# Kernel optimization log

Measured on AMD Instinct MI355X. Metric: run time of the kernel, lower is better.

The kernel has to match this reference:

```python
import jax, jax.numpy as jnp
import numpy as np

D_MODEL = 512
N_HEADS = 8
NUM_NODES = 20
EPS = 1e-5

def _layer_norm(x, g, b):
    mu = jnp.mean(x, axis=-1, keepdims=True)
    var = jnp.var(x, axis=-1, keepdims=True)
    return (x - mu) * jax.lax.rsqrt(var + EPS) * g + b

def _conv1d(x_bcn, w_oik):
    # x: [B, C, N], w: [O, I, K], padding = K//2 (same)
    k = w_oik.shape[-1]
    p = k // 2
    return jax.lax.conv_general_dilated(
        x_bcn, w_oik, window_strides=(1,), padding=[(p, p)],
        dimension_numbers=('NCH', 'OIH', 'NCH'))

def setup_inputs() -> dict:
    key = jax.random.key(0)
    ks = jax.random.split(key, 6)
    B, N, D, H = 4096, NUM_NODES, D_MODEL, N_HEADS
    x = jax.random.normal(ks[0], (B, N, D), dtype=jnp.float32)
    s = 1.0 / np.sqrt(D * 3)
    Wq = jax.random.normal(ks[1], (D, D, 3), dtype=jnp.float32) * s
    Wk = jax.random.normal(ks[2], (D, D, 3), dtype=jnp.float32) * s
    Wv = jax.random.normal(ks[3], (D, D, 3), dtype=jnp.float32) * s
    rel_table = jax.random.normal(ks[4], (2 * N - 1, H), dtype=jnp.float32) * 0.02
    Wo = jax.random.normal(ks[5], (D, D), dtype=jnp.float32) * (1.0 / np.sqrt(D))
    bo = jnp.zeros((D,), dtype=jnp.float32)
    ones = jnp.ones((D,), dtype=jnp.float32)
    zeros = jnp.zeros((D,), dtype=jnp.float32)
    return {"x": x, "Wq": Wq, "Wk": Wk, "Wv": Wv,
            "lnq_g": ones, "lnq_b": zeros, "lnk_g": ones, "lnk_b": zeros,
            "lnv_g": ones, "lnv_b": zeros,
            "rel_table": rel_table, "Wo": Wo, "bo": bo}

def reference(x, Wq, Wk, Wv, lnq_g, lnq_b, lnk_g, lnk_b, lnv_g, lnv_b, rel_table, Wo, bo):
    B, N, D = x.shape
    H = N_HEADS
    dk = D // H
    x_p = jnp.transpose(x, (0, 2, 1))  # [B, D, N]

    def proj(W, g, b):
        c = _conv1d(x_p, W)                      # [B, D, N]
        c = _layer_norm(jnp.transpose(c, (0, 2, 1)), g, b)  # [B, N, D]
        return x + c                              # residual

    q = proj(Wq, lnq_g, lnq_b)
    k = proj(Wk, lnk_g, lnk_b)
    v = proj(Wv, lnv_g, lnv_b)

    q = q.reshape(B, N, H, dk).transpose(0, 2, 1, 3)  # [B,H,N,dk]
    k = k.reshape(B, N, H, dk).transpose(0, 2, 1, 3)
    v = v.reshape(B, N, H, dk).transpose(0, 2, 1, 3)

    scale = 1.0 / np.sqrt(dk)
    scores = jnp.einsum('bhnd,bhmd->bhnm', q, k) * scale  # [B,H,N,N]

    # relative position bias: index[i,j] = i - j + N - 1
    coords = jnp.arange(N)
    rel_idx = coords[:, None] - coords[None, :] + (N - 1)   # [N,N]
    rel_bias = rel_table[rel_idx]                            # [N,N,H]
    rel_bias = jnp.transpose(rel_bias, (2, 0, 1))[None]      # [1,H,N,N]
    scores = scores + rel_bias

    attn = jax.nn.softmax(scores, axis=-1)
    out = jnp.einsum('bhnm,bhmd->bhnd', attn, v)             # [B,H,N,dk]
    out = out.transpose(0, 2, 1, 3).reshape(B, N, D)
    return out @ Wo.T + bo
```

## Files before the change

kernel.cpp:

```cpp
#include <hip/hip_runtime.h>
#include <hip/hip_bf16.h>
#include <stdint.h>
#include <string.h>

typedef __attribute__((ext_vector_type(8))) __bf16 bf16x8;
typedef __attribute__((ext_vector_type(4))) __bf16 bf16x4;
typedef __attribute__((ext_vector_type(4))) float f32x4;
typedef __attribute__((ext_vector_type(16))) float f32x16;

#define B_TOT   4096
#define NN      20
#define DM      512
#define NC1     1536
#define M_TOT   (B_TOT*NN)
#define NPAD    22

__device__ __forceinline__ void async_copy16(const __bf16* g, __bf16* l) {
    __builtin_amdgcn_global_load_lds(
        (__attribute__((address_space(1))) void*)g,
        (__attribute__((address_space(3))) void*)l, 16, 0, 0);
}

template<typename T>
__device__ __forceinline__ void load8(const T* p, float* r) {
    if constexpr (sizeof(T) == 4) {
        f32x4 a = *(const f32x4*)p;
        f32x4 b = *(const f32x4*)(p + 4);
#pragma unroll
        for (int i = 0; i < 4; ++i) { r[i] = a[i]; r[i + 4] = b[i]; }
    } else {
        bf16x8 a = *(const bf16x8*)p;
#pragma unroll
        for (int i = 0; i < 8; ++i) r[i] = (float)a[i];
    }
}

__device__ __forceinline__ bf16x8 zero8() {
    bf16x8 z;
#pragma unroll
    for (int i = 0; i < 8; ++i) z[i] = (__bf16)0.f;
    return z;
}

__device__ __forceinline__ uint32_t pkbf(float a, float b) {
    __bf16 x = (__bf16)a, y = (__bf16)b;
    uint16_t ux, uy;
    __builtin_memcpy(&ux, &x, 2); __builtin_memcpy(&uy, &y, 2);
    return (uint32_t)ux | ((uint32_t)uy << 16);
}

__device__ __forceinline__ bf16x8 mkfrag(uint32_t w0, uint32_t w1, uint32_t w2, uint32_t w3) {
    union { uint32_t u[4]; bf16x8 v; } X;
    X.u[0] = w0; X.u[1] = w1; X.u[2] = w2; X.u[3] = w3;
    return X.v;
}

__global__ void detect_kernel(const uint32_t* __restrict__ xw, int* __restrict__ mode) {
    int lane = threadIdx.x & 63;
    int susp = 0;
#pragma unroll
    for (int i = 0; i < 4; ++i) {
        uint32_t w = xw[lane * 4 + i];
        uint32_t e = (w >> 7) & 0xFF;
        if ((e >= 118 && e <= 130) || (w & 0xFFFFu) == 0) susp++;
    }
#pragma unroll
    for (int o = 32; o > 0; o >>= 1) susp += __shfl_xor(susp, o, 64);
    if (lane == 0) *mode = (susp > 128) ? 1 : 0;
}

template<typename T>
__device__ __forceinline__ void wt_body(
    const T* __restrict__ Wq, const T* __restrict__ Wk, const T* __restrict__ Wv,
    const T* __restrict__ Wo, __bf16* __restrict__ Wt, __bf16* __restrict__ Wob, int t)
{
    if (t < 3 * 512 * 512) {
        int p = t >> 18;
        int r = t & 262143;
        int o = r >> 9, i = r & 511;
        const T* W = (p == 0) ? Wq : ((p == 1) ? Wk : Wv);
        const T* src = W + (size_t)(o * 512 + i) * 3;
        float w0 = (float)src[0], w1 = (float)src[1], w2 = (float)src[2];
        size_t base = (size_t)(p * 512 + o) * 1536 + i;
        Wt[base]        = (__bf16)w0;
        Wt[base + 512]  = (__bf16)w1;
        Wt[base + 1024] = (__bf16)w2;
    } else {
        int g2 = t - 3 * 512 * 512;
        Wob[g2] = (__bf16)(float)Wo[g2];
    }
}

__global__ __launch_bounds__(256) void wt_kernel(
    const void* Wq, const void* Wk, const void* Wv, const void* Wo,
    __bf16* Wt, __bf16* Wob, const int* mode)
{
    int t = blockIdx.x * 256 + threadIdx.x;
    if (*mode)
        wt_body<__bf16>((const __bf16*)Wq, (const __bf16*)Wk, (const __bf16*)Wv,
                        (const __bf16*)Wo, Wt, Wob, t);
    else
        wt_body<float>((const float*)Wq, (const float*)Wk, (const float*)Wv,
                       (const float*)Wo, Wt, Wob, t);
}

template<typename T>
__device__ __forceinline__ void xpad_body(
    const T* __restrict__ x, __bf16* __restrict__ xp, int idx)
{
    int col = (idx & 63) * 8;
    int row = idx >> 6;
    int b = row / 22;
    int np = row - b * 22;
    bf16x8 ov;
    if (np == 0 || np == 21) {
        ov = zero8();
    } else {
        float tmp[8];
        load8<T>(x + ((size_t)(b * 20 + np - 1) * 512 + col), tmp);
#pragma unroll
        for (int t = 0; t < 8; ++t) ov[t] = (__bf16)tmp[t];
    }
    *(bf16x8*)(xp + (size_t)row * 512 + col) = ov;
}

__global__ __launch_bounds__(256) void xpad_kernel(
    const void* x, __bf16* xp, const int* mode)
{
    int idx = blockIdx.x * 256 + threadIdx.x;
    if (*mode) xpad_body<__bf16>((const __bf16*)x, xp, idx);
    else       xpad_body<float>((const float*)x, xp, idx);
}

#define SBAR()  __builtin_amdgcn_s_barrier()
#define SCHED0() __builtin_amdgcn_sched_barrier(0)
#define LGKM0() do { asm volatile("s_waitcnt lgkmcnt(0)" ::: "memory"); SCHED0(); } while (0)
#define VM4()   do { SCHED0(); asm volatile("s_waitcnt vmcnt(4)" ::: "memory"); } while (0)
#define VM0()   do { SCHED0(); asm volatile("s_waitcnt vmcnt(0)" ::: "memory"); } while (0)

__device__ __forceinline__ void g1_loadA(const __bf16* slab, int off, bf16x8 (&aq)[4]) {
#pragma unroll
    for (int i = 0; i < 4; ++i) aq[i] = *(const bf16x8*)(slab + off + i * 512);
}
__device__ __forceinline__ void g1_loadB(const __bf16* slab, int off, bf16x8 (&bq)[4]) {
#pragma unroll
    for (int i = 0; i < 4; ++i) bq[i] = *(const bf16x8*)(slab + off + i * 512);
}
template<int QM>
__device__ __forceinline__ void g1_mma(bf16x8 (&aq)[4], bf16x8 (&bq)[4], f32x4 (&acc)[8][4]) {
    __builtin_amdgcn_s_setprio(1);
#pragma unroll
    for (int i = 0; i < 4; ++i)
#pragma unroll
        for (int nf = 0; nf < 4; ++nf)
            acc[QM * 4 + i][nf] = __builtin_amdgcn_mfma_f32_16x16x32_bf16(
                aq[i], bq[nf], acc[QM * 4 + i][nf], 0, 0, 0);
    __builtin_amdgcn_s_setprio(0);
}

template<int NT>
__device__ __forceinline__ void kloop8(
    const __bf16* aP0, const __bf16* aP1, const __bf16* bP0, const __bf16* bP1,
    __bf16* shA, __bf16* shB, int sdst, int rdA, int rdB, f32x4 (&acc)[8][4])
{
    bf16x8 aq[4], bq[4];
    { __bf16* d = shA + 0 * 8192 + sdst; async_copy16(aP0 + 0, d);  async_copy16(aP1 + 0, d + 4096); }
    { __bf16* d = shB + 0 * 8192 + sdst; async_copy16(bP0 + 0, d);  async_copy16(bP1 + 0, d + 4096); }
    { __bf16* d = shA + 1 * 8192 + sdst; async_copy16(aP0 + 32, d); async_copy16(aP1 + 32, d + 4096); }
    { __bf16* d = shB + 1 * 8192 + sdst; async_copy16(bP0 + 32, d); async_copy16(bP1 + 32, d + 4096); }
    VM4();
    SBAR();

    for (int t = 0; t < NT; ++t) {
        const int cur = t & 1;
        const __bf16* A0 = shA + (cur * 2 + 0) * 8192;
        const __bf16* A1 = shA + (cur * 2 + 1) * 8192;
        const __bf16* B0 = shB + (cur * 2 + 0) * 8192;
        const __bf16* B1 = shB + (cur * 2 + 1) * 8192;
        __bf16* dA0 = shA + ((cur ^ 1) * 2 + 0) * 8192 + sdst;
        __bf16* dA1 = shA + ((cur ^ 1) * 2 + 1) * 8192 + sdst;
        __bf16* dB0 = shB + ((cur ^ 1) * 2 + 0) * 8192 + sdst;
        __bf16* dB1 = shB + ((cur ^ 1) * 2 + 1) * 8192 + sdst;
        const int kn = (t + 1) * 64;
        const bool st = (t < NT - 1);

        g1_loadA(A0, rdA, aq);
        g1_loadB(B0, rdB, bq);
        if (st) { async_copy16(aP0 + kn, dA0); async_copy16(aP1 + kn, dA0 + 4096); }
        SBAR(); LGKM0();
        g1_mma<0>(aq, bq, acc);
        SBAR();

        g1_loadA(A0, rdA + 2048, aq);
        if (st) { async_copy16(bP0 + kn, dB0); async_copy16(bP1 + kn, dB0 + 4096); }
        if (st) VM4(); else VM0();
        SBAR(); LGKM0();
        g1_mma<1>(aq, bq, acc);
        SBAR();

        g1_loadA(A1, rdA, aq);
        g1_loadB(B1, rdB, bq);
        if (st) { async_copy16(aP0 + kn + 32, dA1); async_copy16(aP1 + kn + 32, dA1 + 4096); }
        SBAR(); LGKM0();
        g1_mma<0>(aq, bq, acc);
        SBAR();

        g1_loadA(A1, rdA + 2048, aq);
        if (st) { async_copy16(bP0 + kn + 32, dB1); async_copy16(bP1 + kn + 32, dB1 + 4096); }
        if (st) VM4();
        SBAR(); LGKM0();
        g1_mma<1>(aq, bq, acc);
        SBAR();
    }
}

__global__ __launch_bounds__(512, 2) void g1_kernel(
    const __bf16* __restrict__ xpad, const __bf16* __restrict__ Wt,
    __bf16* __restrict__ Cout, int mbase)
{
    extern __shared__ __align__(16) __bf16 sh[];
    __bf16* shA = sh;
    __bf16* shB = sh + 32768;

    const int tid = threadIdx.x;
    const int w = tid >> 6, l = tid & 63;
    const int lr = l & 15, lq = l >> 4;
    const int wm = w >> 2, wn = w & 3;

    int nwg = gridDim.x;
    int bid = blockIdx.x;
    if ((nwg & 7) == 0) bid = (bid & 7) * (nwg >> 3) + (bid >> 3);
    const int nb = bid % 6;
    const int mb = bid / 6;
    const int n0 = nb * 256;
    const int mloc = mb * 256;

    const int rin = l >> 2;
    const int pc  = (l & 3) * 8;
    const int lc  = (rin >= 8) ? (pc ^ 16) : pc;
    const int R0 = w * 16 + rin;
    const int R1 = 128 + R0;
    const int g0 = mbase + mloc + R0, g1r = mbase + mloc + R1;
    const __bf16* aP0 = xpad + (size_t)((g0 / 20) * 22 + g0 % 20) * 512 + lc;
    const __bf16* aP1 = xpad + (size_t)((g1r / 20) * 22 + g1r % 20) * 512 + lc;
    const __bf16* bP0 = Wt + (size_t)(n0 + R0) * 1536 + lc;
    const __bf16* bP1 = Wt + (size_t)(n0 + R1) * 1536 + lc;
    const int sdst = w * 512 + l * 8;

    const int swzcol = (lr >= 8) ? ((lq * 8) ^ 16) : (lq * 8);
    const int ardoff = lr * 32 + swzcol;
    const int rdA = wm * 8 * 512 + ardoff;
    const int rdB = wn * 4 * 512 + ardoff;

    f32x4 acc[8][4] = {};
    kloop8<24>(aP0, aP1, bP0, bP1, shA, shB, sdst, rdA, rdB, acc);

#pragma unroll
    for (int mf = 0; mf < 8; ++mf) {
#pragma unroll
        for (int r = 0; r < 4; ++r) {
            int row = mloc + wm * 128 + mf * 16 + lq * 4 + r;
            size_t base = (size_t)row * 1536 + n0 + wn * 64 + lr;
#pragma unroll
            for (int nf = 0; nf < 4; ++nf)
                Cout[base + nf * 16] = (__bf16)acc[mf][nf][r];
        }
    }
}

template<typename T>
__device__ __forceinline__ void attn_body(
    const __bf16* __restrict__ xpad, const __bf16* __restrict__ cqkv,
    const T* __restrict__ lnq_g, const T* __restrict__ lnq_b,
    const T* __restrict__ lnk_g, const T* __restrict__ lnk_b,
    const T* __restrict__ lnv_g, const T* __restrict__ lnv_b,
    const T* __restrict__ rel, __bf16* __restrict__ aout, int bbase,
    __bf16* sq , __bf16* vT ,
    float* rbt )
{
    const int tid = threadIdx.x;
    const int wave = tid >> 6, lane = tid & 63;
    const int bl = blockIdx.x;
    char* sqb = (char*)sq;
    char* vTb = (char*)vT;
    const size_t xpbase = ((size_t)(bbase + bl) * NPAD + 1) * DM;
    const size_t cbase = (size_t)bl * NN * NC1;

#pragma unroll
    for (int k = 0; k < 4; ++k)
        *(bf16x8*)(vTb + tid * 64 + k * 16) = zero8();
    if (tid < 312) {
        int h = tid & 7, d = tid >> 3;
        rbt[h * 40 + d] = (float)rel[tid];
    }
    __syncthreads();

#pragma unroll
    for (int rr = 0; rr < 8; ++rr) {
        int row = wave + rr * 8;
        if (row < 60) {
            int p = row / 20;
            int n = row - p * 20;
            bf16x8 cv = *(const bf16x8*)(cqkv + cbase + (size_t)n * NC1 + p * 512 + lane * 8);
            bf16x8 xv = *(const bf16x8*)(xpad + xpbase + (size_t)n * DM + lane * 8);
            float vals[8]; float s1 = 0.f, s2 = 0.f;
#pragma unroll
            for (int t = 0; t < 8; ++t) { float f = (float)cv[t]; vals[t] = f; s1 += f; s2 += f * f; }
#pragma unroll
            for (int o = 32; o > 0; o >>= 1) { s1 += __shfl_xor(s1, o, 64); s2 += __shfl_xor(s2, o, 64); }
            float mu = s1 * (1.f / 512.f);
            float var = s2 * (1.f / 512.f) - mu * mu;
            float rs = rsqrtf(var + 1e-5f);
            const T* g  = (p == 0) ? lnq_g : (p == 1) ? lnk_g : lnv_g;
            const T* bb = (p == 0) ? lnq_b : (p == 1) ? lnk_b : lnv_b;
            float gv[8], bv[8];
            load8<T>(g  + lane * 8, gv);
            load8<T>(bb + lane * 8, bv);
            bf16x8 ov;
#pragma unroll
            for (int t = 0; t < 8; ++t)
                ov[t] = (__bf16)((vals[t] - mu) * rs * gv[t] + bv[t] + (float)xv[t]);
            if (p < 2) {
                *(bf16x8*)(sqb + row * 1024 + ((lane * 16) ^ ((row & 7) << 4))) = ov;
            } else {
#pragma unroll
                for (int t = 0; t < 8; ++t) {
                    int c = lane * 8 + t;
                    unsigned short ub;
                    __bf16 b = ov[t];
                    __builtin_memcpy(&ub, &b, 2);
                    *(unsigned short*)(vTb + c * 64 + ((n * 2) ^ (((c >> 3) & 3) << 4))) = ub;
                }
            }
        }
    }
    __syncthreads();

    const int h  = wave;
    const int ic = lane & 31;
    const int lq = lane >> 5;

    f32x16 s;
#pragma unroll
    for (int r = 0; r < 16; ++r) s[r] = 0.f;
#pragma unroll
    for (int call = 0; call < 4; ++call) {
        int kb2 = (call * 16 + lq * 8) * 2;
        bf16x8 af = zero8(), bf_ = zero8();
        if (ic < 20) {
            int rk = 20 + ic;
            af  = *(const bf16x8*)(sqb + rk * 1024 + ((h * 128 + kb2) ^ ((rk & 7) << 4)));
            bf_ = *(const bf16x8*)(sqb + ic * 1024 + ((h * 128 + kb2) ^ ((ic & 7) << 4)));
        }
        s = __builtin_amdgcn_mfma_f32_32x32x16_bf16(af, bf_, s, 0, 0, 0);
    }
    __syncthreads();

    {
        float mx = -1e30f;
#pragma unroll
        for (int r = 0; r < 16; ++r) {
            int j = (r & 3) + 8 * (r >> 2) + 4 * lq;
            if (j < 20) {
                int d = ic - j + 19;
                d = d < 0 ? 0 : (d > 38 ? 38 : d);
                s[r] = s[r] * 0.125f + rbt[h * 40 + d];
                mx = fmaxf(mx, s[r]);
            } else s[r] = -1e30f;
        }
        mx = fmaxf(mx, __shfl_xor(mx, 32, 64));
        float sum = 0.f;
#pragma unroll
        for (int r = 0; r < 16; ++r) {
            int j = (r & 3) + 8 * (r >> 2) + 4 * lq;
            float e = (j < 20) ? __expf(s[r] - mx) : 0.f;
            s[r] = e; sum += e;
        }
        sum += __shfl_xor(sum, 32, 64);
        float inv = 1.f / sum;
#pragma unroll
        for (int r = 0; r < 16; ++r) s[r] *= inv;
    }

    bf16x8 pa1, pa2;
    {
        uint32_t pk[8], qk[8];
#pragma unroll
        for (int k = 0; k < 8; ++k) pk[k] = pkbf(s[2 * k], s[2 * k + 1]);
#pragma unroll
        for (int k = 0; k < 8; ++k) qk[k] = (uint32_t)__shfl_xor((int)pk[k], 32, 64);
        pa1 = lq ? mkfrag(qk[2], qk[3], pk[2], pk[3]) : mkfrag(pk[0], pk[1], qk[0], qk[1]);
        pa2 = lq ? mkfrag(qk[6], qk[7], pk[6], pk[7]) : mkfrag(pk[4], pk[5], qk[4], qk[5]);
    }

#pragma unroll 1
    for (int ct = 0; ct < 2; ++ct) {
        const int cb0 = h * 64 + ct * 32;
        const int c_a = cb0 + ic;
        const int arow = c_a * 64;
        const int aswz = ((c_a >> 3) & 3) << 4;
        bf16x8 a1 = *(const bf16x8*)(vTb + arow + ((lq * 16 + 0)  ^ aswz));
        bf16x8 a2 = *(const bf16x8*)(vTb + arow + ((lq * 16 + 32) ^ aswz));
        f32x16 o;
#pragma unroll
        for (int r = 0; r < 16; ++r) o[r] = 0.f;
        o = __builtin_amdgcn_mfma_f32_32x32x16_bf16(a1, pa1, o, 0, 0, 0);
        o = __builtin_amdgcn_mfma_f32_32x32x16_bf16(a2, pa2, o, 0, 0, 0);
        if (ic < 20) {
#pragma unroll
            for (int g2 = 0; g2 < 4; ++g2) {
                int c0 = cb0 + 8 * g2 + 4 * lq;
                bf16x4 ov4;
#pragma unroll
                for (int e = 0; e < 4; ++e) ov4[e] = (__bf16)o[g2 * 4 + e];
                *(bf16x4*)(sqb + ic * 1024 + ((c0 * 2) ^ ((ic & 7) << 4))) = ov4;
            }
        }
    }
    __syncthreads();

    __bf16* ab = aout + (size_t)bl * NN * DM;
    for (int t = tid; t < 1280; t += 512) {
        int row = t >> 6;
        int bc = (t & 63) * 16;
        bf16x8 vv = *(const bf16x8*)(sqb + row * 1024 + (bc ^ ((row & 7) << 4)));
        *(bf16x8*)(ab + t * 8) = vv;
    }
}

__global__ __launch_bounds__(512, 4) void attn_kernel(
    const __bf16* xpad, const __bf16* cqkv,
    const void* lnq_g, const void* lnq_b, const void* lnk_g, const void* lnk_b,
    const void* lnv_g, const void* lnv_b, const void* rel,
    __bf16* aout, int bbase, const int* mode)
{
    __shared__ __align__(16) __bf16 sq[40 * 512];
    __shared__ __align__(16) __bf16 vT[512 * 32];
    __shared__ float rbt[8 * 40];
    if (*mode)
        attn_body<__bf16>(xpad, cqkv,
            (const __bf16*)lnq_g, (const __bf16*)lnq_b, (const __bf16*)lnk_g,
            (const __bf16*)lnk_b, (const __bf16*)lnv_g, (const __bf16*)lnv_b,
            (const __bf16*)rel, aout, bbase, sq, vT, rbt);
    else
        attn_body<float>(xpad, cqkv,
            (const float*)lnq_g, (const float*)lnq_b, (const float*)lnk_g,
            (const float*)lnk_b, (const float*)lnv_g, (const float*)lnv_b,
            (const float*)rel, aout, bbase, sq, vT, rbt);
}

template<typename T>
__device__ __forceinline__ void g3_body(
    const __bf16* __restrict__ Ain, const __bf16* __restrict__ Wob,
    const T* __restrict__ bo, T* __restrict__ out, int mbase, __bf16* sh)
{
    __bf16* shA = sh;
    __bf16* shB = sh + 32768;

    const int tid = threadIdx.x;
    const int w = tid >> 6, l = tid & 63;
    const int lr = l & 15, lq = l >> 4;
    const int wm = w >> 2, wn = w & 3;

    int nwg = gridDim.x;
    int bid = blockIdx.x;
    if ((nwg & 7) == 0) bid = (bid & 7) * (nwg >> 3) + (bid >> 3);
    const int nb = bid & 1;
    const int mb = bid >> 1;
    const int n0 = nb * 256;
    const int mloc = mb * 256;

    const int rin = l >> 2;
    const int pc  = (l & 3) * 8;
    const int lc  = (rin >= 8) ? (pc ^ 16) : pc;
    const int R0 = w * 16 + rin;
    const int R1 = 128 + R0;
    const __bf16* aP0 = Ain + (size_t)(mloc + R0) * 512 + lc;
    const __bf16* aP1 = Ain + (size_t)(mloc + R1) * 512 + lc;
    const __bf16* bP0 = Wob + (size_t)(n0 + R0) * 512 + lc;
    const __bf16* bP1 = Wob + (size_t)(n0 + R1) * 512 + lc;
    const int sdst = w * 512 + l * 8;

    const int swzcol = (lr >= 8) ? ((lq * 8) ^ 16) : (lq * 8);
    const int ardoff = lr * 32 + swzcol;
    const int rdA = wm * 8 * 512 + ardoff;
    const int rdB = wn * 4 * 512 + ardoff;

    f32x4 acc[8][4] = {};
    kloop8<8>(aP0, aP1, bP0, bP1, shA, shB, sdst, rdA, rdB, acc);

    float bias[4];
#pragma unroll
    for (int nf = 0; nf < 4; ++nf) bias[nf] = (float)bo[n0 + wn * 64 + lr + nf * 16];
#pragma unroll
    for (int mf = 0; mf < 8; ++mf) {
#pragma unroll
        for (int r = 0; r < 4; ++r) {
            int row = mloc + wm * 128 + mf * 16 + lq * 4 + r;
            size_t gbase = (size_t)(mbase + row) * 512 + n0 + wn * 64 + lr;
#pragma unroll
            for (int nf = 0; nf < 4; ++nf)
                out[gbase + nf * 16] = (T)(acc[mf][nf][r] + bias[nf]);
        }
    }
}

__global__ __launch_bounds__(512, 2) void g3_kernel(
    const __bf16* Ain, const __bf16* Wob, const void* bo, void* out,
    int mbase, const int* mode)
{
    extern __shared__ __align__(16) __bf16 sh3[];
    if (*mode) g3_body<__bf16>(Ain, Wob, (const __bf16*)bo, (__bf16*)out, mbase, sh3);
    else       g3_body<float>(Ain, Wob, (const float*)bo, (float*)out, mbase, sh3);
}

extern "C" void kernel_launch(void* const* d_in, const int* in_sizes, int n_in,
                              void* d_out, int out_size, void* d_ws, size_t ws_size,
                              hipStream_t stream) {
    (void)in_sizes; (void)n_in; (void)out_size; (void)ws_size;
    char* ws = (char*)d_ws;
    int*    mode = (int*)ws;
    __bf16* Wt   = (__bf16*)(ws + 256);
    __bf16* Wob  = (__bf16*)(ws + 256 + 4718592);
    __bf16* xpad = (__bf16*)(ws + 256 + 4718592 + 524288);
    const size_t off_c = 256 + 4718592 + 524288 + (size_t)B_TOT * NPAD * DM * 2;

    static bool attr_set = false;
    if (!attr_set) {
        (void)hipFuncSetAttribute((const void*)g1_kernel,
                                  hipFuncAttributeMaxDynamicSharedMemorySize, 131072);
        (void)hipFuncSetAttribute((const void*)g3_kernel,
                                  hipFuncAttributeMaxDynamicSharedMemorySize, 131072);
        attr_set = true;
    }

    __bf16* Cbuf = (__bf16*)(ws + off_c);
    __bf16* Abuf = (__bf16*)(ws + off_c + (size_t)M_TOT * NC1 * 2);

    detect_kernel<<<dim3(1), dim3(64), 0, stream>>>((const uint32_t*)d_in[0], mode);
    wt_kernel<<<dim3(4096), dim3(256), 0, stream>>>(
        d_in[1], d_in[2], d_in[3], d_in[11], Wt, Wob, mode);
    xpad_kernel<<<dim3(22528), dim3(256), 0, stream>>>(d_in[0], xpad, mode);

    g1_kernel<<<dim3(6 * (M_TOT / 256)), dim3(512), 131072, stream>>>(
        xpad, Wt, Cbuf, 0);
    attn_kernel<<<dim3(B_TOT), dim3(512), 0, stream>>>(
        xpad, Cbuf, d_in[4], d_in[5], d_in[6], d_in[7], d_in[8], d_in[9],
        d_in[10], Abuf, 0, mode);
    g3_kernel<<<dim3(2 * (M_TOT / 256)), dim3(512), 131072, stream>>>(
        Abuf, Wob, d_in[12], d_out, 0, mode);
}
```

Before: 834.5 us.

## Fuse output projection into attention kernel, removing separate GEMM launch

The Wo projection plus bias is now computed inside the attention kernel with MFMA. Each block multiplies its 20x512 attention output, still in LDS, by Wo rows read directly from global memory and writes the final output. This drops the intermediate attention buffer round-trip and one kernel launch. In exchange, Wo fragments are re-read from global/L2 by every block without LDS tiling, and the 32-row MFMA tile leaves 12 of its rows unused.

```diff
diff --git a/kernel.cpp b/kernel.cpp
--- a/kernel.cpp
+++ b/kernel.cpp
@@ -274,7 +274,8 @@
     const T* __restrict__ lnq_g, const T* __restrict__ lnq_b,
     const T* __restrict__ lnk_g, const T* __restrict__ lnk_b,
     const T* __restrict__ lnv_g, const T* __restrict__ lnv_b,
-    const T* __restrict__ rel, __bf16* __restrict__ aout, int bbase,
+    const T* __restrict__ rel, const __bf16* __restrict__ Wob,
+    const T* __restrict__ bo, T* __restrict__ out,
     __bf16* sq , __bf16* vT ,
     float* rbt )
 {
@@ -283,7 +284,7 @@
     const int bl = blockIdx.x;
     char* sqb = (char*)sq;
     char* vTb = (char*)vT;
-    const size_t xpbase = ((size_t)(bbase + bl) * NPAD + 1) * DM;
+    const size_t xpbase = ((size_t)bl * NPAD + 1) * DM;
     const size_t cbase = (size_t)bl * NN * NC1;
 
 #pragma unroll
@@ -419,12 +420,28 @@
     }
     __syncthreads();
 
-    __bf16* ab = aout + (size_t)bl * NN * DM;
-    for (int t = tid; t < 1280; t += 512) {
-        int row = t >> 6;
-        int bc = (t & 63) * 16;
-        bf16x8 vv = *(const bf16x8*)(sqb + row * 1024 + (bc ^ ((row & 7) << 4)));
-        *(bf16x8*)(ab + t * 8) = vv;
+    T* outp = out + (size_t)bl * NN * DM;
+#pragma unroll 1
+    for (int cg = 0; cg < 2; ++cg) {
+        const int oc0 = h * 64 + cg * 32;
+        const float bias_v = (float)bo[oc0 + ic];
+        const __bf16* wsrc = Wob + (size_t)(oc0 + ic) * 512;
+        f32x16 o;
+#pragma unroll
+        for (int r = 0; r < 16; ++r) o[r] = 0.f;
+#pragma unroll 4
+        for (int ks = 0; ks < 32; ++ks) {
+            bf16x8 af = *(const bf16x8*)(sqb + ic * 1024 +
+                            ((ks * 32 + lq * 16) ^ ((ic & 7) << 4)));
+            bf16x8 bf_ = *(const bf16x8*)(wsrc + ks * 16 + lq * 8);
+            o = __builtin_amdgcn_mfma_f32_32x32x16_bf16(af, bf_, o, 0, 0, 0);
+        }
+#pragma unroll
+        for (int r = 0; r < 16; ++r) {
+            int i = (r & 3) + 8 * (r >> 2) + 4 * lq;
+            if (i < 20)
+                outp[(size_t)i * DM + oc0 + ic] = (T)(o[r] + bias_v);
+        }
     }
 }
 
@@ -432,7 +449,7 @@
     const __bf16* xpad, const __bf16* cqkv,
     const void* lnq_g, const void* lnq_b, const void* lnk_g, const void* lnk_b,
     const void* lnv_g, const void* lnv_b, const void* rel,
-    __bf16* aout, int bbase, const int* mode)
+    const __bf16* Wob, const void* bo, void* out, const int* mode)
 {
     __shared__ __align__(16) __bf16 sq[40 * 512];
     __shared__ __align__(16) __bf16 vT[512 * 32];
@@ -441,77 +458,12 @@
         attn_body<__bf16>(xpad, cqkv,
             (const __bf16*)lnq_g, (const __bf16*)lnq_b, (const __bf16*)lnk_g,
             (const __bf16*)lnk_b, (const __bf16*)lnv_g, (const __bf16*)lnv_b,
-            (const __bf16*)rel, aout, bbase, sq, vT, rbt);
+            (const __bf16*)rel, Wob, (const __bf16*)bo, (__bf16*)out, sq, vT, rbt);
     else
         attn_body<float>(xpad, cqkv,
             (const float*)lnq_g, (const float*)lnq_b, (const float*)lnk_g,
             (const float*)lnk_b, (const float*)lnv_g, (const float*)lnv_b,
-            (const float*)rel, aout, bbase, sq, vT, rbt);
-}
-
-template<typename T>
-__device__ __forceinline__ void g3_body(
-    const __bf16* __restrict__ Ain, const __bf16* __restrict__ Wob,
-    const T* __restrict__ bo, T* __restrict__ out, int mbase, __bf16* sh)
-{
-    __bf16* shA = sh;
-    __bf16* shB = sh + 32768;
-
-    const int tid = threadIdx.x;
-    const int w = tid >> 6, l = tid & 63;
-    const int lr = l & 15, lq = l >> 4;
-    const int wm = w >> 2, wn = w & 3;
-
-    int nwg = gridDim.x;
-    int bid = blockIdx.x;
-    if ((nwg & 7) == 0) bid = (bid & 7) * (nwg >> 3) + (bid >> 3);
-    const int nb = bid & 1;
-    const int mb = bid >> 1;
-    const int n0 = nb * 256;
-    const int mloc = mb * 256;
-
-    const int rin = l >> 2;
-    const int pc  = (l & 3) * 8;
-    const int lc  = (rin >= 8) ? (pc ^ 16) : pc;
-    const int R0 = w * 16 + rin;
-    const int R1 = 128 + R0;
-    const __bf16* aP0 = Ain + (size_t)(mloc + R0) * 512 + lc;
-    const __bf16* aP1 = Ain + (size_t)(mloc + R1) * 512 + lc;
-    const __bf16* bP0 = Wob + (size_t)(n0 + R0) * 512 + lc;
-    const __bf16* bP1 = Wob + (size_t)(n0 + R1) * 512 + lc;
-    const int sdst = w * 512 + l * 8;
-
-    const int swzcol = (lr >= 8) ? ((lq * 8) ^ 16) : (lq * 8);
-    const int ardoff = lr * 32 + swzcol;
-    const int rdA = wm * 8 * 512 + ardoff;
-    const int rdB = wn * 4 * 512 + ardoff;
-
-    f32x4 acc[8][4] = {};
-    kloop8<8>(aP0, aP1, bP0, bP1, shA, shB, sdst, rdA, rdB, acc);
-
-    float bias[4];
-#pragma unroll
-    for (int nf = 0; nf < 4; ++nf) bias[nf] = (float)bo[n0 + wn * 64 + lr + nf * 16];
-#pragma unroll
-    for (int mf = 0; mf < 8; ++mf) {
-#pragma unroll
-        for (int r = 0; r < 4; ++r) {
-            int row = mloc + wm * 128 + mf * 16 + lq * 4 + r;
-            size_t gbase = (size_t)(mbase + row) * 512 + n0 + wn * 64 + lr;
-#pragma unroll
-            for (int nf = 0; nf < 4; ++nf)
-                out[gbase + nf * 16] = (T)(acc[mf][nf][r] + bias[nf]);
-        }
-    }
-}
-
-__global__ __launch_bounds__(512, 2) void g3_kernel(
-    const __bf16* Ain, const __bf16* Wob, const void* bo, void* out,
-    int mbase, const int* mode)
-{
-    extern __shared__ __align__(16) __bf16 sh3[];
-    if (*mode) g3_body<__bf16>(Ain, Wob, (const __bf16*)bo, (__bf16*)out, mbase, sh3);
-    else       g3_body<float>(Ain, Wob, (const float*)bo, (float*)out, mbase, sh3);
+            (const float*)rel, Wob, (const float*)bo, (float*)out, sq, vT, rbt);
 }
 
 extern "C" void kernel_launch(void* const* d_in, const int* in_sizes, int n_in,
@@ -529,13 +481,10 @@
     if (!attr_set) {
         (void)hipFuncSetAttribute((const void*)g1_kernel,
                                   hipFuncAttributeMaxDynamicSharedMemorySize, 131072);
-        (void)hipFuncSetAttribute((const void*)g3_kernel,
-                                  hipFuncAttributeMaxDynamicSharedMemorySize, 131072);
         attr_set = true;
     }
 
     __bf16* Cbuf = (__bf16*)(ws + off_c);
-    __bf16* Abuf = (__bf16*)(ws + off_c + (size_t)M_TOT * NC1 * 2);
 
     detect_kernel<<<dim3(1), dim3(64), 0, stream>>>((const uint32_t*)d_in[0], mode);
     wt_kernel<<<dim3(4096), dim3(256), 0, stream>>>(
@@ -546,7 +495,5 @@
         xpad, Wt, Cbuf, 0);
     attn_kernel<<<dim3(B_TOT), dim3(512), 0, stream>>>(
         xpad, Cbuf, d_in[4], d_in[5], d_in[6], d_in[7], d_in[8], d_in[9],
-        d_in[10], Abuf, 0, mode);
-    g3_kernel<<<dim3(2 * (M_TOT / 256)), dim3(512), 131072, stream>>>(
-        Abuf, Wob, d_in[12], d_out, 0, mode);
-}
+        d_in[10], Wob, d_in[12], d_out, mode);
+}
```

New measurement: 986.2 us. 18.2% more time.
